# Kernel tuning notes

Measured on AMD Instinct MI355X. Metric: run time of the kernel, lower is better.

Reference implementation:

```python
import jax, jax.numpy as jnp
import numpy as np

N_NODES = 50000
N_EDGES = 800000
IN_FEATS = 128
N_HIDDEN = 128
N_CLASSES = 64


def setup_inputs() -> dict:
    key = jax.random.key(0)
    ks = jax.random.split(key, 12)
    x = jax.random.normal(ks[0], (N_NODES, IN_FEATS), dtype=jnp.float32)
    src = jax.random.randint(ks[1], (N_EDGES,), 0, N_NODES, dtype=jnp.int32)
    dst = jax.random.randint(ks[2], (N_EDGES,), 0, N_NODES, dtype=jnp.int32)
    dims = [(IN_FEATS, N_HIDDEN), (N_HIDDEN, N_HIDDEN), (N_HIDDEN, N_CLASSES)]
    inp = {"x": x, "src": src, "dst": dst}
    for i, (din, dout) in enumerate(dims):
        s = (2.0 / (din + dout)) ** 0.5  # xavier-ish init scale
        inp[f"Wself{i}"] = jax.random.normal(ks[3 + 3 * i], (din, dout), dtype=jnp.float32) * s
        inp[f"Wneigh{i}"] = jax.random.normal(ks[4 + 3 * i], (din, dout), dtype=jnp.float32) * s
        inp[f"b{i}"] = jnp.zeros((dout,), dtype=jnp.float32)
    return inp


def _sage_conv(h, src, dst, inv_deg, Wself, Wneigh, b):
    # mean aggregation over in-neighbors: gather on src, segment-sum on dst
    agg = jax.ops.segment_sum(h[src], dst, num_segments=N_NODES)  # [N, d]
    h_neigh = agg * inv_deg[:, None]
    return h @ Wself + h_neigh @ Wneigh + b


def reference(x, src, dst, Wself0, Wneigh0, b0, Wself1, Wneigh1, b1, Wself2, Wneigh2, b2):
    # in-degree (clamped to 1, matching DGL mean aggregator), shared across layers
    deg = jax.ops.segment_sum(jnp.ones((N_EDGES,), dtype=jnp.float32), dst, num_segments=N_NODES)
    inv_deg = 1.0 / jnp.maximum(deg, 1.0)
    # dropout is identity in eval mode
    h = _sage_conv(x, src, dst, inv_deg, Wself0, Wneigh0, b0)
    h = jax.nn.relu(h)
    h = _sage_conv(h, src, dst, inv_deg, Wself1, Wneigh1, b1)
    h = jax.nn.relu(h)
    h = _sage_conv(h, src, dst, inv_deg, Wself2, Wneigh2, b2)
    return h
```

## Files before the change

kernel.cpp:

```cpp
#include <hip/hip_runtime.h>

#define N_NODES 50000
#define N_EDGES 800000
#define NB_SCAN 196

typedef unsigned short ushort_t;
typedef __attribute__((ext_vector_type(8))) short  short8v;
typedef __attribute__((ext_vector_type(4))) float  float4v;
typedef __attribute__((ext_vector_type(4))) unsigned short ushort4v;
typedef __attribute__((ext_vector_type(8))) unsigned short ushort8v;
typedef __attribute__((ext_vector_type(4))) int int4v;

__device__ __forceinline__ ushort_t f2bf(float f) {
    unsigned u = __float_as_uint(f);
    unsigned r = 0x7fffu + ((u >> 16) & 1u);
    return (ushort_t)((u + r) >> 16);
}
__device__ __forceinline__ float bf2f(ushort_t h) {
    return __uint_as_float((unsigned)h << 16);
}

__global__ __launch_bounds__(256) void cast_zero_k(const float* __restrict__ x,
                                                   ushort_t* __restrict__ xb,
                                                   int* __restrict__ deg, int n4) {
    int i = blockIdx.x * 256 + threadIdx.x;
    if (i < n4) {
        float4 v = ((const float4*)x)[i];
        ushort4v h;
        h[0] = f2bf(v.x); h[1] = f2bf(v.y); h[2] = f2bf(v.z); h[3] = f2bf(v.w);
        ((ushort4v*)xb)[i] = h;
    }
    if (i < N_NODES) deg[i] = 0;
}

__global__ __launch_bounds__(256) void deg_count_k(const int4v* __restrict__ dst4,
                                                   int* __restrict__ deg) {
    const int grp = blockIdx.x & 7;
    const int lo = grp * 6250, hi = lo + 6250;
    const int stride = (gridDim.x >> 3) * 256;
    const int n4 = N_EDGES / 4;
    for (int i = (blockIdx.x >> 3) * 256 + threadIdx.x; i < n4; i += stride) {
        int4v d = __builtin_nontemporal_load(dst4 + i);
        if (d[0] >= lo && d[0] < hi) atomicAdd(deg + d[0], 1);
        if (d[1] >= lo && d[1] < hi) atomicAdd(deg + d[1], 1);
        if (d[2] >= lo && d[2] < hi) atomicAdd(deg + d[2], 1);
        if (d[3] >= lo && d[3] < hi) atomicAdd(deg + d[3], 1);
    }
}


__global__ __launch_bounds__(256) void block_sum_k(const int* __restrict__ deg,
                                                   int* __restrict__ bsum, int n) {
    __shared__ int s[256];
    int t = threadIdx.x, b = blockIdx.x;
    int i = b * 256 + t;
    s[t] = (i < n) ? deg[i] : 0;
    __syncthreads();
#pragma unroll
    for (int off = 128; off > 0; off >>= 1) {
        if (t < off) s[t] += s[t + off];
        __syncthreads();
    }
    if (t == 0) bsum[b] = s[0];
}

__global__ __launch_bounds__(256) void scan_bsum_k(const int* __restrict__ bsum,
                                                   int* __restrict__ boff,
                                                   int* __restrict__ rowptr_last, int nb) {
    __shared__ int s[256];
    int t = threadIdx.x;
    int v = (t < nb) ? bsum[t] : 0;
    s[t] = v;
    __syncthreads();
#pragma unroll
    for (int off = 1; off < 256; off <<= 1) {
        int u = (t >= off) ? s[t - off] : 0;
        __syncthreads();
        s[t] += u;
        __syncthreads();
    }
    if (t < nb) boff[t] = s[t] - v;
    if (t == 255) *rowptr_last = s[255];
}

__global__ __launch_bounds__(256) void write_rowptr_k(const int* __restrict__ deg,
                                                      const int* __restrict__ boff,
                                                      int* __restrict__ rowptr,
                                                      int* __restrict__ cursor,
                                                      float* __restrict__ inv, int n) {
    __shared__ int s[256];
    int t = threadIdx.x, b = blockIdx.x;
    int i = b * 256 + t;
    int d = (i < n) ? deg[i] : 0;
    s[t] = d;
    __syncthreads();
#pragma unroll
    for (int off = 1; off < 256; off <<= 1) {
        int u = (t >= off) ? s[t - off] : 0;
        __syncthreads();
        s[t] += u;
        __syncthreads();
    }
    if (i < n) {
        int r = boff[b] + s[t] - d;
        rowptr[i] = r;
        cursor[i] = r;
        inv[i] = 1.0f / fmaxf((float)d, 1.0f);
    }
}

__global__ __launch_bounds__(256) void scatter_k(const int4v* __restrict__ src4,
                                                 const int4v* __restrict__ dst4,
                                                 int* __restrict__ cursor,
                                                 int* __restrict__ csr) {
    const int grp = blockIdx.x & 7;
    const int lo = grp * 6250, hi = lo + 6250;
    const int stride = (gridDim.x >> 3) * 256;
    const int n4 = N_EDGES / 4;
    for (int i = (blockIdx.x >> 3) * 256 + threadIdx.x; i < n4; i += stride) {
        int4v d = __builtin_nontemporal_load(dst4 + i);
        int4v sv = __builtin_nontemporal_load(src4 + i);
        if (d[0] >= lo && d[0] < hi) csr[atomicAdd(cursor + d[0], 1)] = sv[0];
        if (d[1] >= lo && d[1] < hi) csr[atomicAdd(cursor + d[1], 1)] = sv[1];
        if (d[2] >= lo && d[2] < hi) csr[atomicAdd(cursor + d[2], 1)] = sv[2];
        if (d[3] >= lo && d[3] < hi) csr[atomicAdd(cursor + d[3], 1)] = sv[3];
    }
}

__global__ __launch_bounds__(256) void pack_all_k(const float* __restrict__ W0n, const float* __restrict__ W0s,
                                                  const float* __restrict__ W1n, const float* __restrict__ W1s,
                                                  const float* __restrict__ W2n, const float* __restrict__ W2s,
                                                  ushort_t* __restrict__ P) {
    int tid = blockIdx.x * 256 + threadIdx.x;
    const float* W; int dout; int base; int r;
    if      (tid < 2048)  { W = W0n; dout = 128; base = 0;     r = tid; }
    else if (tid < 4096)  { W = W0s; dout = 128; base = 16384; r = tid - 2048; }
    else if (tid < 6144)  { W = W1n; dout = 128; base = 32768; r = tid - 4096; }
    else if (tid < 8192)  { W = W1s; dout = 128; base = 49152; r = tid - 6144; }
    else if (tid < 9216)  { W = W2n; dout = 64;  base = 65536; r = tid - 8192; }
    else                  { W = W2s; dout = 64;  base = 73728; r = tid - 9216; }
    int lane = r & 63;
    int ks = (r >> 6) & 3;
    int nt = r >> 8;
    int col = nt * 16 + (lane & 15);
    int k0 = ks * 32 + ((lane >> 4) << 3);
    ushort_t* d = P + (size_t)base + (size_t)r * 8;
    ushort4v lo4, hi4;
#pragma unroll
    for (int j = 0; j < 4; ++j) lo4[j] = f2bf(W[(size_t)(k0 + j) * dout + col]);
#pragma unroll
    for (int j = 0; j < 4; ++j) hi4[j] = f2bf(W[(size_t)(k0 + 4 + j) * dout + col]);
    *(ushort4v*)d = lo4;
    *(ushort4v*)(d + 4) = hi4;
}

__global__ __launch_bounds__(256) void aggm_k(const ushort_t* __restrict__ h,
                                              const int* __restrict__ rowptr,
                                              const int* __restrict__ csr,
                                              const float* __restrict__ inv,
                                              ushort_t* __restrict__ m, int N) {
    int node = (blockIdx.x * 256 + threadIdx.x) >> 4;
    int c = threadIdx.x & 15;
    if (node >= N) return;
    int start = rowptr[node], end = rowptr[node + 1];

    const ushort8v* hp = (const ushort8v*)h;
    float a0[8] = {}, a1[8] = {}, a2[8] = {}, a3[8] = {};
    int j = start;
    for (; j + 3 < end; j += 4) {
        int u0 = csr[j], u1 = csr[j + 1], u2 = csr[j + 2], u3 = csr[j + 3];
        ushort8v w0 = hp[(size_t)u0 * 16 + c];
        ushort8v w1 = hp[(size_t)u1 * 16 + c];
        ushort8v w2 = hp[(size_t)u2 * 16 + c];
        ushort8v w3 = hp[(size_t)u3 * 16 + c];
#pragma unroll
        for (int k = 0; k < 8; ++k) {
            a0[k] += bf2f(w0[k]); a1[k] += bf2f(w1[k]);
            a2[k] += bf2f(w2[k]); a3[k] += bf2f(w3[k]);
        }
    }
    for (; j < end; ++j) {
        ushort8v w = hp[(size_t)csr[j] * 16 + c];
#pragma unroll
        for (int k = 0; k < 8; ++k) a0[k] += bf2f(w[k]);
    }
    float s = inv[node];
    ushort8v o;
#pragma unroll
    for (int k = 0; k < 8; ++k) o[k] = f2bf(((a0[k] + a1[k]) + (a2[k] + a3[k])) * s);
    ((ushort8v*)m)[(size_t)node * 16 + c] = o;
}

__global__ __launch_bounds__(256, 4) void fusedgemm_k(const ushort_t* __restrict__ H,
                                                      const ushort_t* __restrict__ M,
                                                      const short8v* __restrict__ Ws,
                                                      const short8v* __restrict__ Wn,
                                                      const float* __restrict__ bias,
                                                      ushort_t* __restrict__ Out, int N) {
    __shared__ ushort_t sm[2][64 * 128];
    char* sbH = (char*)sm[0];
    char* sbM = (char*)sm[1];
    const int bm = blockIdx.x * 64;
    const int t = threadIdx.x;
    const int w = t >> 6, l = t & 63;

    {
        const ushort8v* Hp = (const ushort8v*)H;
        const ushort8v* Mp = (const ushort8v*)M;
        ushort8v zeroV = {0, 0, 0, 0, 0, 0, 0, 0};
#pragma unroll
        for (int it = 0; it < 4; ++it) {
            int r = it * 16 + (t >> 4);
            int row = bm + r;
            int byte = (r * 256 + (t & 15) * 16) ^ ((r & 7) << 4);
            ushort8v vh = zeroV, vm = zeroV;
            if (row < N) {
                vh = Hp[(size_t)row * 16 + (t & 15)];
                vm = Mp[(size_t)row * 16 + (t & 15)];
            }
            *(ushort8v*)(sbH + byte) = vh;
            *(ushort8v*)(sbM + byte) = vm;
        }
    }
    __syncthreads();

    float bv[8];
#pragma unroll
    for (int nt = 0; nt < 8; ++nt) bv[nt] = bias[nt * 16 + (l & 15)];

    float4v acc[8] = {};
#pragma unroll
    for (int ks = 0; ks < 4; ++ks) {
        int r0 = w * 16 + (l & 15);
        int b0 = (r0 * 256 + ks * 64 + (l >> 4) * 16) ^ ((r0 & 7) << 4);
        short8v ah = *(const short8v*)(sbH + b0);
        short8v am = *(const short8v*)(sbM + b0);
#pragma unroll
        for (int nt = 0; nt < 8; ++nt) {
            short8v bs = Ws[(nt * 4 + ks) * 64 + l];
            short8v bn = Wn[(nt * 4 + ks) * 64 + l];
            acc[nt] = __builtin_amdgcn_mfma_f32_16x16x32_bf16(ah, bs, acc[nt], 0, 0, 0);
            acc[nt] = __builtin_amdgcn_mfma_f32_16x16x32_bf16(am, bn, acc[nt], 0, 0, 0);
        }
    }

#pragma unroll
    for (int i = 0; i < 4; ++i) {
        int row = bm + w * 16 + (l >> 4) * 4 + i;
        if (row < N) {
#pragma unroll
            for (int nt = 0; nt < 8; ++nt) {
                int col = nt * 16 + (l & 15);
                Out[(size_t)row * 128 + col] = f2bf(fmaxf(acc[nt][i] + bv[nt], 0.f));
            }
        }
    }
}

__global__ __launch_bounds__(256, 4) void dual64_k(const ushort_t* __restrict__ A,
                                                   const short8v* __restrict__ Wn,
                                                   const short8v* __restrict__ Ws,
                                                   const float* __restrict__ bias,
                                                   ushort_t* __restrict__ Z,
                                                   float* __restrict__ S, int N) {
    constexpr int NT = 4;
    __shared__ ushort_t Asm[64 * 128];
    char* sb = (char*)Asm;
    const int bm = blockIdx.x * 64;
    const int t = threadIdx.x;
    const int w = t >> 6, l = t & 63;

    {
        const ushort8v* Ap = (const ushort8v*)A;
        ushort8v zeroV = {0, 0, 0, 0, 0, 0, 0, 0};
#pragma unroll
        for (int it = 0; it < 4; ++it) {
            int r = it * 16 + (t >> 4);
            int row = bm + r;
            ushort8v v = zeroV;
            if (row < N) v = Ap[(size_t)row * 16 + (t & 15)];
            int byte = (r * 256 + (t & 15) * 16) ^ ((r & 7) << 4);
            *(ushort8v*)(sb + byte) = v;
        }
    }
    __syncthreads();

    float bv[NT];
#pragma unroll
    for (int nt = 0; nt < NT; ++nt) bv[nt] = bias[nt * 16 + (l & 15)];

    float4v accS[NT] = {}, accN[NT] = {};
#pragma unroll
    for (int ks = 0; ks < 4; ++ks) {
        int r0 = w * 16 + (l & 15);
        int b0 = (r0 * 256 + ks * 64 + (l >> 4) * 16) ^ ((r0 & 7) << 4);
        short8v a = *(const short8v*)(sb + b0);
#pragma unroll
        for (int nt = 0; nt < NT; ++nt) {
            short8v bs = Ws[(nt * 4 + ks) * 64 + l];
            short8v bn = Wn[(nt * 4 + ks) * 64 + l];
            accS[nt] = __builtin_amdgcn_mfma_f32_16x16x32_bf16(a, bs, accS[nt], 0, 0, 0);
            accN[nt] = __builtin_amdgcn_mfma_f32_16x16x32_bf16(a, bn, accN[nt], 0, 0, 0);
        }
    }

#pragma unroll
    for (int i = 0; i < 4; ++i) {
        int row = bm + w * 16 + (l >> 4) * 4 + i;
        if (row < N) {
#pragma unroll
            for (int nt = 0; nt < NT; ++nt) {
                int col = nt * 16 + (l & 15);
                S[(size_t)row * 64 + col] = accS[nt][i] + bv[nt];
                Z[(size_t)row * 64 + col] = f2bf(accN[nt][i]);
            }
        }
    }
}

__global__ __launch_bounds__(256) void agg64_k(const ushort_t* __restrict__ z,
                                               const int* __restrict__ rowptr,
                                               const int* __restrict__ csr,
                                               const float* __restrict__ inv,
                                               float* __restrict__ out, int N) {
    int node = (blockIdx.x * 256 + threadIdx.x) >> 3;
    int c = threadIdx.x & 7;
    if (node >= N) return;
    int start = rowptr[node], end = rowptr[node + 1];

    const ushort8v* zp = (const ushort8v*)z;
    float a0[8] = {}, a1[8] = {}, a2[8] = {}, a3[8] = {};
    int j = start;
    for (; j + 3 < end; j += 4) {
        int u0 = csr[j], u1 = csr[j + 1], u2 = csr[j + 2], u3 = csr[j + 3];
        ushort8v w0 = zp[(size_t)u0 * 8 + c];
        ushort8v w1 = zp[(size_t)u1 * 8 + c];
        ushort8v w2 = zp[(size_t)u2 * 8 + c];
        ushort8v w3 = zp[(size_t)u3 * 8 + c];
#pragma unroll
        for (int k = 0; k < 8; ++k) {
            a0[k] += bf2f(w0[k]); a1[k] += bf2f(w1[k]);
            a2[k] += bf2f(w2[k]); a3[k] += bf2f(w3[k]);
        }
    }
    for (; j < end; ++j) {
        ushort8v w = zp[(size_t)csr[j] * 8 + c];
#pragma unroll
        for (int k = 0; k < 8; ++k) a0[k] += bf2f(w[k]);
    }
    float s = inv[node];
    float* op = out + (size_t)node * 64 + c * 8;
    float4 o0 = *(float4*)op;
    float4 o1 = *(float4*)(op + 4);
    o0.x += ((a0[0] + a1[0]) + (a2[0] + a3[0])) * s;
    o0.y += ((a0[1] + a1[1]) + (a2[1] + a3[1])) * s;
    o0.z += ((a0[2] + a1[2]) + (a2[2] + a3[2])) * s;
    o0.w += ((a0[3] + a1[3]) + (a2[3] + a3[3])) * s;
    o1.x += ((a0[4] + a1[4]) + (a2[4] + a3[4])) * s;
    o1.y += ((a0[5] + a1[5]) + (a2[5] + a3[5])) * s;
    o1.z += ((a0[6] + a1[6]) + (a2[6] + a3[6])) * s;
    o1.w += ((a0[7] + a1[7]) + (a2[7] + a3[7])) * s;
    *(float4*)op = o0;
    *(float4*)(op + 4) = o1;
}


extern "C" void kernel_launch(void* const* d_in, const int* in_sizes, int n_in,
                              void* d_out, int out_size, void* d_ws, size_t ws_size,
                              hipStream_t stream) {
    const float* x       = (const float*)d_in[0];
    const int*   src     = (const int*)d_in[1];
    const int*   dst     = (const int*)d_in[2];
    const float* Wself0  = (const float*)d_in[3];
    const float* Wneigh0 = (const float*)d_in[4];
    const float* b0      = (const float*)d_in[5];
    const float* Wself1  = (const float*)d_in[6];
    const float* Wneigh1 = (const float*)d_in[7];
    const float* b1      = (const float*)d_in[8];
    const float* Wself2  = (const float*)d_in[9];
    const float* Wneigh2 = (const float*)d_in[10];
    const float* b2      = (const float*)d_in[11];
    float* out = (float*)d_out;

    char* ws = (char*)d_ws;
    size_t off = 0;
    auto alloc = [&](size_t bytes) -> void* {
        void* p = ws + off;
        off += (bytes + 255) & ~(size_t)255;
        return p;
    };
    int*      deg    = (int*)alloc((size_t)N_NODES * 4);
    float*    inv    = (float*)alloc((size_t)N_NODES * 4);
    int*      rowptr = (int*)alloc((size_t)(N_NODES + 1) * 4);
    int*      cursor = (int*)alloc((size_t)N_NODES * 4);
    int*      csr    = (int*)alloc((size_t)N_EDGES * 4);
    int*      bsum   = (int*)alloc((size_t)NB_SCAN * 4);
    int*      boff   = (int*)alloc((size_t)NB_SCAN * 4);
    ushort_t* packW  = (ushort_t*)alloc((size_t)81920 * 2);
    ushort_t* xb     = (ushort_t*)alloc((size_t)N_NODES * 128 * 2);
    ushort_t* mbuf   = (ushort_t*)alloc((size_t)N_NODES * 128 * 2);
    ushort_t* h1     = (ushort_t*)alloc((size_t)N_NODES * 128 * 2);
    ushort_t* h2     = (ushort_t*)alloc((size_t)N_NODES * 128 * 2);
    ushort_t* z64    = (ushort_t*)alloc((size_t)N_NODES * 64 * 2);

    dim3 b256(256);
    const int gemmBlocks  = (N_NODES + 63) / 64;
    const int aggmBlocks  = (N_NODES * 16 + 255) / 256;
    const int agg64Blocks = (N_NODES * 8 + 255) / 256;
    const int castBlocks  = (N_NODES * 32 + 255) / 256;

    cast_zero_k<<<castBlocks, b256, 0, stream>>>(x, xb, deg, N_NODES * 32);
    deg_count_k<<<1024, b256, 0, stream>>>((const int4v*)dst, deg);
    block_sum_k<<<NB_SCAN, b256, 0, stream>>>(deg, bsum, N_NODES);
    scan_bsum_k<<<1, b256, 0, stream>>>(bsum, boff, rowptr + N_NODES, NB_SCAN);
    write_rowptr_k<<<NB_SCAN, b256, 0, stream>>>(deg, boff, rowptr, cursor, inv, N_NODES);
    scatter_k<<<1024, b256, 0, stream>>>((const int4v*)src, (const int4v*)dst, cursor, csr);

    pack_all_k<<<40, b256, 0, stream>>>(Wneigh0, Wself0, Wneigh1, Wself1, Wneigh2, Wself2, packW);
    const short8v* pN0 = (const short8v*)(packW);
    const short8v* pS0 = (const short8v*)(packW + 16384);
    const short8v* pN1 = (const short8v*)(packW + 32768);
    const short8v* pS1 = (const short8v*)(packW + 49152);
    const short8v* pN2 = (const short8v*)(packW + 65536);
    const short8v* pS2 = (const short8v*)(packW + 73728);

    aggm_k<<<aggmBlocks, b256, 0, stream>>>(xb, rowptr, csr, inv, mbuf, N_NODES);
    fusedgemm_k<<<gemmBlocks, b256, 0, stream>>>(xb, mbuf, pS0, pN0, b0, h1, N_NODES);

    aggm_k<<<aggmBlocks, b256, 0, stream>>>(h1, rowptr, csr, inv, mbuf, N_NODES);
    fusedgemm_k<<<gemmBlocks, b256, 0, stream>>>(h1, mbuf, pS1, pN1, b1, h2, N_NODES);

    dual64_k<<<gemmBlocks, b256, 0, stream>>>(h2, pN2, pS2, b2, z64, out, N_NODES);
    agg64_k<<<agg64Blocks, b256, 0, stream>>>(z64, rowptr, csr, inv, out, N_NODES);
}
```

Before: 222.3 us.

## Pre-bucket edges by destination group before degree count and CSR scatter

Adds a bucketing pass that partitions edges into 8 destination-range buckets of (dst,src) pairs using shared-memory counters and one global atomic per group per block. The degree-count and scatter kernels then read only their group's bucket instead of each of 8 block groups scanning the full edge list and filtering. This cuts redundant edge reads roughly eightfold, at the cost of an extra kernel and writing and reading an 8-byte-per-edge bucket buffer. Bucket capacity is fixed at 131072 per group, which holds for uniformly random destinations but would overflow under heavy skew.

```diff
diff --git a/kernel.cpp b/kernel.cpp
--- a/kernel.cpp
+++ b/kernel.cpp
@@ -3,6 +3,8 @@
 #define N_NODES 50000
 #define N_EDGES 800000
 #define NB_SCAN 196
+#define NODES_PER_GRP 6250
+#define BUCKET_CAP 131072
 
 typedef unsigned short ushort_t;
 typedef __attribute__((ext_vector_type(8))) short  short8v;
@@ -22,7 +24,8 @@
 
 __global__ __launch_bounds__(256) void cast_zero_k(const float* __restrict__ x,
                                                    ushort_t* __restrict__ xb,
-                                                   int* __restrict__ deg, int n4) {
+                                                   int* __restrict__ deg,
+                                                   int* __restrict__ bcur, int n4) {
     int i = blockIdx.x * 256 + threadIdx.x;
     if (i < n4) {
         float4 v = ((const float4*)x)[i];
@@ -31,20 +34,66 @@
         ((ushort4v*)xb)[i] = h;
     }
     if (i < N_NODES) deg[i] = 0;
-}
-
-__global__ __launch_bounds__(256) void deg_count_k(const int4v* __restrict__ dst4,
-                                                   int* __restrict__ deg) {
+    if (i < 8) bcur[i] = 0;
+}
+
+__global__ __launch_bounds__(256) void bucket_k(const int4v* __restrict__ dst4,
+                                                const int4v* __restrict__ src4,
+                                                int* __restrict__ bcur,
+                                                int2* __restrict__ buckets) {
+    __shared__ int lcount[8];
+    __shared__ int lbase[8];
+    const int t = threadIdx.x, b = blockIdx.x;
+    if (t < 8) lcount[t] = 0;
+    __syncthreads();
+
+    int4v d[4], s[4];
+    const int base4 = b * 1024 + t;
+#pragma unroll
+    for (int i = 0; i < 4; ++i) {
+        int idx = base4 + i * 256;
+        if (idx < N_EDGES / 4) {
+            d[i] = __builtin_nontemporal_load(dst4 + idx);
+            s[i] = __builtin_nontemporal_load(src4 + idx);
+        } else {
+            d[i][0] = d[i][1] = d[i][2] = d[i][3] = -1;
+            s[i][0] = s[i][1] = s[i][2] = s[i][3] = 0;
+        }
+    }
+    int g[16], li[16];
+#pragma unroll
+    for (int i = 0; i < 4; ++i)
+#pragma unroll
+        for (int j = 0; j < 4; ++j) {
+            int e = i * 4 + j;
+            int dv = d[i][j];
+            g[e] = (dv >= 0) ? (dv / NODES_PER_GRP) : -1;
+            li[e] = (g[e] >= 0) ? atomicAdd(&lcount[g[e]], 1) : 0;
+        }
+    __syncthreads();
+    if (t < 8) lbase[t] = atomicAdd(bcur + t, lcount[t]);
+    __syncthreads();
+#pragma unroll
+    for (int i = 0; i < 4; ++i)
+#pragma unroll
+        for (int j = 0; j < 4; ++j) {
+            int e = i * 4 + j;
+            if (g[e] >= 0) {
+                int pos = lbase[g[e]] + li[e];
+                buckets[(size_t)g[e] * BUCKET_CAP + pos] = make_int2(d[i][j], s[i][j]);
+            }
+        }
+}
+
+__global__ __launch_bounds__(256) void deg_bucket_k(const int* __restrict__ bcur,
+                                                    const int2* __restrict__ buckets,
+                                                    int* __restrict__ deg) {
     const int grp = blockIdx.x & 7;
-    const int lo = grp * 6250, hi = lo + 6250;
+    const int cnt = bcur[grp];
+    const int2* bk = buckets + (size_t)grp * BUCKET_CAP;
     const int stride = (gridDim.x >> 3) * 256;
-    const int n4 = N_EDGES / 4;
-    for (int i = (blockIdx.x >> 3) * 256 + threadIdx.x; i < n4; i += stride) {
-        int4v d = __builtin_nontemporal_load(dst4 + i);
-        if (d[0] >= lo && d[0] < hi) atomicAdd(deg + d[0], 1);
-        if (d[1] >= lo && d[1] < hi) atomicAdd(deg + d[1], 1);
-        if (d[2] >= lo && d[2] < hi) atomicAdd(deg + d[2], 1);
-        if (d[3] >= lo && d[3] < hi) atomicAdd(deg + d[3], 1);
+    for (int i = (blockIdx.x >> 3) * 256 + threadIdx.x; i < cnt; i += stride) {
+        atomicAdd(deg + bk[i].x, 1);
     }
 }
 
@@ -109,21 +158,17 @@
     }
 }
 
-__global__ __launch_bounds__(256) void scatter_k(const int4v* __restrict__ src4,
-                                                 const int4v* __restrict__ dst4,
-                                                 int* __restrict__ cursor,
-                                                 int* __restrict__ csr) {
+__global__ __launch_bounds__(256) void scatter_bucket_k(const int* __restrict__ bcur,
+                                                        const int2* __restrict__ buckets,
+                                                        int* __restrict__ cursor,
+                                                        int* __restrict__ csr) {
     const int grp = blockIdx.x & 7;
-    const int lo = grp * 6250, hi = lo + 6250;
+    const int cnt = bcur[grp];
+    const int2* bk = buckets + (size_t)grp * BUCKET_CAP;
     const int stride = (gridDim.x >> 3) * 256;
-    const int n4 = N_EDGES / 4;
-    for (int i = (blockIdx.x >> 3) * 256 + threadIdx.x; i < n4; i += stride) {
-        int4v d = __builtin_nontemporal_load(dst4 + i);
-        int4v sv = __builtin_nontemporal_load(src4 + i);
-        if (d[0] >= lo && d[0] < hi) csr[atomicAdd(cursor + d[0], 1)] = sv[0];
-        if (d[1] >= lo && d[1] < hi) csr[atomicAdd(cursor + d[1], 1)] = sv[1];
-        if (d[2] >= lo && d[2] < hi) csr[atomicAdd(cursor + d[2], 1)] = sv[2];
-        if (d[3] >= lo && d[3] < hi) csr[atomicAdd(cursor + d[3], 1)] = sv[3];
+    for (int i = (blockIdx.x >> 3) * 256 + threadIdx.x; i < cnt; i += stride) {
+        int2 e = bk[i];
+        csr[atomicAdd(cursor + e.x, 1)] = e.y;
     }
 }
 
@@ -389,32 +434,36 @@
         off += (bytes + 255) & ~(size_t)255;
         return p;
     };
-    int*      deg    = (int*)alloc((size_t)N_NODES * 4);
-    float*    inv    = (float*)alloc((size_t)N_NODES * 4);
-    int*      rowptr = (int*)alloc((size_t)(N_NODES + 1) * 4);
-    int*      cursor = (int*)alloc((size_t)N_NODES * 4);
-    int*      csr    = (int*)alloc((size_t)N_EDGES * 4);
-    int*      bsum   = (int*)alloc((size_t)NB_SCAN * 4);
-    int*      boff   = (int*)alloc((size_t)NB_SCAN * 4);
-    ushort_t* packW  = (ushort_t*)alloc((size_t)81920 * 2);
-    ushort_t* xb     = (ushort_t*)alloc((size_t)N_NODES * 128 * 2);
-    ushort_t* mbuf   = (ushort_t*)alloc((size_t)N_NODES * 128 * 2);
-    ushort_t* h1     = (ushort_t*)alloc((size_t)N_NODES * 128 * 2);
-    ushort_t* h2     = (ushort_t*)alloc((size_t)N_NODES * 128 * 2);
-    ushort_t* z64    = (ushort_t*)alloc((size_t)N_NODES * 64 * 2);
+    int*      deg     = (int*)alloc((size_t)N_NODES * 4);
+    float*    inv     = (float*)alloc((size_t)N_NODES * 4);
+    int*      rowptr  = (int*)alloc((size_t)(N_NODES + 1) * 4);
+    int*      cursor  = (int*)alloc((size_t)N_NODES * 4);
+    int*      csr     = (int*)alloc((size_t)N_EDGES * 4);
+    int*      bsum    = (int*)alloc((size_t)NB_SCAN * 4);
+    int*      boff    = (int*)alloc((size_t)NB_SCAN * 4);
+    int*      bcur    = (int*)alloc((size_t)8 * 4);
+    int2*     buckets = (int2*)alloc((size_t)8 * BUCKET_CAP * 8);
+    ushort_t* packW   = (ushort_t*)alloc((size_t)81920 * 2);
+    ushort_t* xb      = (ushort_t*)alloc((size_t)N_NODES * 128 * 2);
+    ushort_t* mbuf    = (ushort_t*)alloc((size_t)N_NODES * 128 * 2);
+    ushort_t* h1      = (ushort_t*)alloc((size_t)N_NODES * 128 * 2);
+    ushort_t* h2      = (ushort_t*)alloc((size_t)N_NODES * 128 * 2);
+    ushort_t* z64     = (ushort_t*)alloc((size_t)N_NODES * 64 * 2);
 
     dim3 b256(256);
-    const int gemmBlocks  = (N_NODES + 63) / 64;
-    const int aggmBlocks  = (N_NODES * 16 + 255) / 256;
-    const int agg64Blocks = (N_NODES * 8 + 255) / 256;
-    const int castBlocks  = (N_NODES * 32 + 255) / 256;
-
-    cast_zero_k<<<castBlocks, b256, 0, stream>>>(x, xb, deg, N_NODES * 32);
-    deg_count_k<<<1024, b256, 0, stream>>>((const int4v*)dst, deg);
+    const int gemmBlocks   = (N_NODES + 63) / 64;
+    const int aggmBlocks   = (N_NODES * 16 + 255) / 256;
+    const int agg64Blocks  = (N_NODES * 8 + 255) / 256;
+    const int castBlocks   = (N_NODES * 32 + 255) / 256;
+    const int bucketBlocks = (N_EDGES + 4095) / 4096;
+
+    cast_zero_k<<<castBlocks, b256, 0, stream>>>(x, xb, deg, bcur, N_NODES * 32);
+    bucket_k<<<bucketBlocks, b256, 0, stream>>>((const int4v*)dst, (const int4v*)src, bcur, buckets);
+    deg_bucket_k<<<512, b256, 0, stream>>>(bcur, buckets, deg);
     block_sum_k<<<NB_SCAN, b256, 0, stream>>>(deg, bsum, N_NODES);
     scan_bsum_k<<<1, b256, 0, stream>>>(bsum, boff, rowptr + N_NODES, NB_SCAN);
     write_rowptr_k<<<NB_SCAN, b256, 0, stream>>>(deg, boff, rowptr, cursor, inv, N_NODES);
-    scatter_k<<<1024, b256, 0, stream>>>((const int4v*)src, (const int4v*)dst, cursor, csr);
+    scatter_bucket_k<<<512, b256, 0, stream>>>(bcur, buckets, cursor, csr);
 
     pack_all_k<<<40, b256, 0, stream>>>(Wneigh0, Wself0, Wneigh1, Wself1, Wneigh2, Wself2, packW);
     const short8v* pN0 = (const short8v*)(packW);
```

After: 220.5 us. Within noise of the previous version (-0.8%).
